# Optimization experiments

Measured on AMD Instinct MI355X. Metric: run time of the kernel, lower is better.

The kernel has to match this reference:

```python
import jax, jax.numpy as jnp
import numpy as np

ALPHA = 0.2  # LeakyReLU slope
S1, S2 = 5, 10  # neighbor sample sizes, hard-coded in the torch forward

N, F, D, C, B = 100000, 512, 256, 40, 16384


def setup_inputs() -> dict:
    key = jax.random.key(0)
    ks = jax.random.split(key, 7)
    x = jax.random.normal(ks[0], (N, F), dtype=jnp.float32)
    # xavier-like scaling for the weights
    W1 = jax.random.normal(ks[1], (D, F), dtype=jnp.float32) * (2.0 / (D + F)) ** 0.5
    W2 = jax.random.normal(ks[2], (D, D), dtype=jnp.float32) * (2.0 / (D + D)) ** 0.5
    Wc = jax.random.normal(ks[3], (C, D), dtype=jnp.float32) * (2.0 / (C + D)) ** 0.5
    nodes = jax.random.randint(ks[4], (B,), 0, N, dtype=jnp.int32)
    neigh1 = jax.random.randint(ks[5], (N, S1), 0, N, dtype=jnp.int32)
    neigh2 = jax.random.randint(ks[6], (B, S2), 0, N, dtype=jnp.int32)
    return {"x": x, "W1": W1, "W2": W2, "Wc": Wc,
            "nodes": nodes, "neigh1": neigh1, "neigh2": neigh2}


def leaky_relu(v):
    return jnp.where(v >= 0, v, ALPHA * v)


def reference(x, W1, W2, Wc, nodes, neigh1, neigh2):
    # Layer 1 (MeanAggregator, gcn=True): mean over sampled neighbors + self,
    # then linear transform + LeakyReLU. Computed for all N nodes.
    agg1 = (x[neigh1].sum(axis=1) + x) / (S1 + 1)          # [N, F]
    h1 = leaky_relu(agg1 @ W1.T)                            # [N, D]
    # Layer 2: mean over sampled neighbors + self, on batch nodes.
    agg2 = (h1[neigh2].sum(axis=1) + h1[nodes]) / (S2 + 1)  # [B, D]
    h2 = leaky_relu(agg2 @ W2.T)                            # [B, D]
    # scores = self.weight.mm(x_2.t()).t()
    scores = h2 @ Wc.T                                      # [B, C]
    return scores
```

## Files before the change

### kernel.cpp

```cpp
#include <hip/hip_runtime.h>
#include <hip/hip_bf16.h>


#define NN 100000
#define FF 512
#define DD 256
#define BB 16384
#define CC 40

typedef __attribute__((ext_vector_type(8))) short bf16x8;
typedef __attribute__((ext_vector_type(4))) float f32x4;
typedef unsigned short u16;
typedef unsigned int u32;

__device__ __forceinline__ float bf_lo(u32 u) { u32 v = u << 16; float f; __builtin_memcpy(&f, &v, 4); return f; }
__device__ __forceinline__ float bf_hi(u32 u) { u32 v = u & 0xffff0000u; float f; __builtin_memcpy(&f, &v, 4); return f; }
__device__ __forceinline__ float2 bf2f(u32 u) { return make_float2(bf_lo(u), bf_hi(u)); }
__device__ __forceinline__ u32 packbf2(float a, float b) {
  __hip_bfloat162 h = __float22bfloat162_rn(make_float2(a, b));
  u32 u; __builtin_memcpy(&u, &h, 4); return u;
}
__device__ __forceinline__ u16 fbits(float v) {
  __hip_bfloat16 h = __float2bfloat16(v);
  u16 u; __builtin_memcpy(&u, &h, 2); return u;
}
__device__ __forceinline__ float lrelu(float v) { return v >= 0.f ? v : 0.2f * v; }
__device__ __forceinline__ int swz(int r, int c) { return r * 128 + ((c ^ (r & 7)) << 4); }
__device__ __forceinline__ void gld_lds16(const u16* g, void* l) {
  __builtin_amdgcn_global_load_lds((const __attribute__((address_space(1))) unsigned int*)g,
                                   (__attribute__((address_space(3))) unsigned int*)l, 16, 0, 0);
}

__global__ __launch_bounds__(256) void k0_cvt(
    const float* __restrict__ W1, const float* __restrict__ W2, const float* __restrict__ Wc,
    u16* __restrict__ w1b, u16* __restrict__ w2b, u16* __restrict__ wcb)
{
  const int i = blockIdx.x * 256 + threadIdx.x;
  const float* src; u16* dst; int r, cc, rowE;
  if (i < 16384)      { src = W1; dst = w1b; r = i >> 6; cc = i & 63; rowE = 512; }
  else if (i < 24576) { int j = i - 16384; src = W2; dst = w2b; r = j >> 5; cc = j & 31; rowE = 256; }
  else if (i < 25856) { int j = i - 24576; src = Wc; dst = wcb; r = j >> 5; cc = j & 31; rowE = 256; }
  else return;
  const int g = cc >> 3, cp = cc & 7;
  const float* s = src + (u32)r * rowE + g * 64 + (u32)(cp ^ (r & 7)) * 8;
  const float4 v0 = *(const float4*)s;
  const float4 v1 = *(const float4*)(s + 4);
  uint4 o;
  o.x = packbf2(v0.x, v0.y); o.y = packbf2(v0.z, v0.w);
  o.z = packbf2(v1.x, v1.y); o.w = packbf2(v1.z, v1.w);
  *(uint4*)(dst + (u32)r * rowE + g * 64 + cp * 8) = o;
}

__global__ __launch_bounds__(512, 4) void k1_gemm(
    const float* __restrict__ x, const u16* __restrict__ w1b, u16* __restrict__ z)
{
  __shared__ __align__(16) unsigned char lds[49152];

  const int t = threadIdx.x;
  const int rowBase = blockIdx.x * 128;
  const int lane = t & 63, w = t >> 6;
  const int wm = w >> 2, wn = w & 3;
  const int lr = lane & 15, kg = lane >> 4;

  u32 offA[2]; int aW[2];
#pragma unroll
  for (int i = 0; i < 2; ++i) {
    const int id = t + i * 512;
    const int r = id >> 3, c = id & 7;
    int row = rowBase + r; if (row > NN - 1) row = NN - 1;
    offA[i] = (u32)row * FF + c * 8;
    aW[i] = swz(r, c);
  }
  const u32 bofs = (u32)(w * 8 + (lane >> 3)) * FF + (u32)(lane & 7) * 8;
  unsigned char* bl0 = lds + 16384 + w * 1024;

  int aA[2][4], bA[2][4];
#pragma unroll
  for (int kk = 0; kk < 2; ++kk) {
    const int cb = kk * 4 + kg;
#pragma unroll
    for (int m = 0; m < 4; ++m) aA[kk][m] = swz(wm * 64 + m * 16 + lr, cb);
#pragma unroll
    for (int n = 0; n < 4; ++n) bA[kk][n] = 16384 + swz(wn * 64 + n * 16 + lr, cb);
  }

  f32x4 acc[4][4];
#pragma unroll
  for (int m = 0; m < 4; ++m)
#pragma unroll
    for (int n = 0; n < 4; ++n) acc[m][n] = (f32x4)0.0f;

  float4 pa[2][2];
#pragma unroll
  for (int i = 0; i < 2; ++i) {
    pa[i][0] = *(const float4*)(x + offA[i]);
    pa[i][1] = *(const float4*)(x + offA[i] + 4);
  }

  for (int ks = 0; ks < 8; ++ks) {
    if (ks) __builtin_amdgcn_s_barrier();
#pragma unroll
    for (int i = 0; i < 2; ++i) {
      uint4 o;
      o.x = packbf2(pa[i][0].x, pa[i][0].y); o.y = packbf2(pa[i][0].z, pa[i][0].w);
      o.z = packbf2(pa[i][1].x, pa[i][1].y); o.w = packbf2(pa[i][1].z, pa[i][1].w);
      *(uint4*)(lds + aW[i]) = o;
    }
#pragma unroll
    for (int i = 0; i < 4; ++i)
      gld_lds16(w1b + bofs + (u32)i * 64 * FF + (u32)ks * 64, bl0 + i * 8192);
    __syncthreads();
    if (ks < 7) {
#pragma unroll
      for (int i = 0; i < 2; ++i) {
        pa[i][0] = *(const float4*)(x + offA[i] + (u32)(ks + 1) * 64);
        pa[i][1] = *(const float4*)(x + offA[i] + (u32)(ks + 1) * 64 + 4);
      }
    }
    __builtin_amdgcn_sched_barrier(0);
#pragma unroll
    for (int kk = 0; kk < 2; ++kk) {
      bf16x8 av[4], bv[4];
#pragma unroll
      for (int m = 0; m < 4; ++m) av[m] = *(const bf16x8*)(lds + aA[kk][m]);
#pragma unroll
      for (int n = 0; n < 4; ++n) bv[n] = *(const bf16x8*)(lds + bA[kk][n]);
#pragma unroll
      for (int m = 0; m < 4; ++m)
#pragma unroll
        for (int n = 0; n < 4; ++n)
          acc[m][n] = __builtin_amdgcn_mfma_f32_16x16x32_bf16(av[m], bv[n], acc[m][n], 0, 0, 0);
    }
  }
#pragma unroll
  for (int m = 0; m < 4; ++m) {
    const int r0 = rowBase + wm * 64 + m * 16 + kg * 4;
#pragma unroll
    for (int j = 0; j < 4; ++j)
#pragma unroll
      for (int n = 0; n < 4; ++n)
        z[(u32)(r0 + j) * DD + wn * 64 + n * 16 + lr] = fbits(acc[m][n][j]);
  }
}

__global__ __launch_bounds__(256) void k2_agg1(
    const u16* __restrict__ z, const int* __restrict__ neigh1, u16* __restrict__ h1)
{
  const int t = threadIdx.x;
  const int row = blockIdx.x * 8 + (t >> 5);
  const int ch = t & 31;
  const u32 o0 = (u32)row * DD + ch * 8;
  uint4 a = *(const uint4*)(z + o0);
  float2 s0 = bf2f(a.x), s1 = bf2f(a.y), s2 = bf2f(a.z), s3 = bf2f(a.w);
#pragma unroll
  for (int j = 0; j < 5; ++j) {
    const int idx = neigh1[row * 5 + j];
    const uint4 v = *(const uint4*)(z + (u32)idx * DD + ch * 8);
    s0.x += bf_lo(v.x); s0.y += bf_hi(v.x);
    s1.x += bf_lo(v.y); s1.y += bf_hi(v.y);
    s2.x += bf_lo(v.z); s2.y += bf_hi(v.z);
    s3.x += bf_lo(v.w); s3.y += bf_hi(v.w);
  }
  const float sc = 1.0f / 6.0f;
  uint4 o;
  o.x = packbf2(lrelu(s0.x * sc), lrelu(s0.y * sc));
  o.y = packbf2(lrelu(s1.x * sc), lrelu(s1.y * sc));
  o.z = packbf2(lrelu(s2.x * sc), lrelu(s2.y * sc));
  o.w = packbf2(lrelu(s3.x * sc), lrelu(s3.y * sc));
  *(uint4*)(h1 + o0) = o;
}

__global__ __launch_bounds__(512, 2) void k3_fused(
    const u16* __restrict__ h1, const u16* __restrict__ w2b, const u16* __restrict__ wcb,
    const int* __restrict__ nodes, const int* __restrict__ neigh2, float* __restrict__ out)
{
  __shared__ __align__(16) unsigned char lds[65536];

  const int t = threadIdx.x;
  const int rowBase = blockIdx.x * 64;
  const int lane = t & 63, w = t >> 6;
  const int wm = w >> 2, wn = w & 3;
  const int lr = lane & 15, kg = lane >> 4;

#pragma unroll
  for (int i = 0; i < 3; ++i) {
    const int id = t + i * 512;
    uint4 v = make_uint4(0u, 0u, 0u, 0u);
    if (id < 1280) v = *(const uint4*)(wcb + (u32)id * 8);
    *(uint4*)(lds + 40960 + id * 16) = v;
  }

  const int r = t >> 3, c = t & 7;
  const int b = rowBase + r;
  u32 offA[11];
  offA[0] = (u32)nodes[b] * DD + (u32)c * 8;
#pragma unroll
  for (int j = 0; j < 10; ++j)
    offA[1 + j] = (u32)neigh2[b * 10 + j] * DD + (u32)c * 8;
  const int aW = swz(r, c);

  const u32 bofs = (u32)(w * 8 + (lane >> 3)) * DD + (u32)(lane & 7) * 8;
  unsigned char* bl0 = lds + 8192 + w * 1024;

  int aA[2][2], bA[2][4];
#pragma unroll
  for (int kk = 0; kk < 2; ++kk) {
    const int cb = kk * 4 + kg;
#pragma unroll
    for (int m = 0; m < 2; ++m) aA[kk][m] = swz(wm * 32 + m * 16 + lr, cb);
#pragma unroll
    for (int n = 0; n < 4; ++n) bA[kk][n] = 8192 + swz(wn * 64 + n * 16 + lr, cb);
  }

  f32x4 acc[2][4];
#pragma unroll
  for (int m = 0; m < 2; ++m)
#pragma unroll
    for (int n = 0; n < 4; ++n) acc[m][n] = (f32x4)0.0f;

  uint4 ag[11];
#pragma unroll
  for (int j = 0; j < 11; ++j) ag[j] = *(const uint4*)(h1 + offA[j]);

  for (int ks = 0; ks < 4; ++ks) {
    if (ks) __builtin_amdgcn_s_barrier();
    {
      float2 s0 = make_float2(0.f, 0.f), s1 = make_float2(0.f, 0.f);
      float2 s2 = make_float2(0.f, 0.f), s3 = make_float2(0.f, 0.f);
#pragma unroll
      for (int j = 0; j < 11; ++j) {
        s0.x += bf_lo(ag[j].x); s0.y += bf_hi(ag[j].x);
        s1.x += bf_lo(ag[j].y); s1.y += bf_hi(ag[j].y);
        s2.x += bf_lo(ag[j].z); s2.y += bf_hi(ag[j].z);
        s3.x += bf_lo(ag[j].w); s3.y += bf_hi(ag[j].w);
      }
      const float sc = 1.0f / 11.0f;
      uint4 o;
      o.x = packbf2(s0.x * sc, s0.y * sc);
      o.y = packbf2(s1.x * sc, s1.y * sc);
      o.z = packbf2(s2.x * sc, s2.y * sc);
      o.w = packbf2(s3.x * sc, s3.y * sc);
      *(uint4*)(lds + aW) = o;
    }
#pragma unroll
    for (int i = 0; i < 4; ++i)
      gld_lds16(w2b + bofs + (u32)i * 64 * DD + (u32)ks * 64, bl0 + i * 8192);
    __syncthreads();
    if (ks < 3) {
#pragma unroll
      for (int j = 0; j < 11; ++j)
        ag[j] = *(const uint4*)(h1 + offA[j] + (u32)(ks + 1) * 64);
    }
    __builtin_amdgcn_sched_barrier(0);
#pragma unroll
    for (int kk = 0; kk < 2; ++kk) {
      bf16x8 av[2], bv[4];
#pragma unroll
      for (int m = 0; m < 2; ++m) av[m] = *(const bf16x8*)(lds + aA[kk][m]);
#pragma unroll
      for (int n = 0; n < 4; ++n) bv[n] = *(const bf16x8*)(lds + bA[kk][n]);
#pragma unroll
      for (int m = 0; m < 2; ++m)
#pragma unroll
        for (int n = 0; n < 4; ++n)
          acc[m][n] = __builtin_amdgcn_mfma_f32_16x16x32_bf16(av[m], bv[n], acc[m][n], 0, 0, 0);
    }
  }

  __syncthreads();
#pragma unroll
  for (int m = 0; m < 2; ++m) {
#pragma unroll
    for (int j = 0; j < 4; ++j) {
      const int row = wm * 32 + m * 16 + kg * 4 + j;
#pragma unroll
      for (int n = 0; n < 4; ++n) {
        const int col = wn * 64 + n * 16 + lr;
        const int ch = col >> 3;
        const int pch = (ch & 24) | ((ch ^ row) & 7);
        *(u16*)(lds + row * 512 + pch * 16 + (col & 7) * 2) = fbits(lrelu(acc[m][n][j]));
      }
    }
  }
  __syncthreads();

  if (w < 4) {
    f32x4 acc2[3];
#pragma unroll
    for (int n = 0; n < 3; ++n) acc2[n] = (f32x4)0.0f;
    const int arow = w * 16 + lr;
#pragma unroll
    for (int ks2 = 0; ks2 < 8; ++ks2) {
      const int chb = ks2 * 4 + kg;
      const int pchA = (chb & 24) | ((chb ^ arow) & 7);
      const bf16x8 a = *(const bf16x8*)(lds + arow * 512 + pchA * 16);
#pragma unroll
      for (int n = 0; n < 3; ++n) {
        const int brow = n * 16 + lr;
        const int pchB = (chb & 24) | ((chb ^ brow) & 7);
        const bf16x8 bb = *(const bf16x8*)(lds + 40960 + brow * 512 + pchB * 16);
        acc2[n] = __builtin_amdgcn_mfma_f32_16x16x32_bf16(a, bb, acc2[n], 0, 0, 0);
      }
    }
#pragma unroll
    for (int n = 0; n < 3; ++n) {
      const int col = n * 16 + lr;
      if (col < CC) {
#pragma unroll
        for (int j = 0; j < 4; ++j) {
          const int rr = rowBase + w * 16 + kg * 4 + j;
          out[(u32)rr * CC + col] = acc2[n][j];
        }
      }
    }
  }
}

extern "C" void kernel_launch(void* const* d_in, const int* in_sizes, int n_in,
                              void* d_out, int out_size, void* d_ws, size_t ws_size,
                              hipStream_t stream) {
  const float* x    = (const float*)d_in[0];
  const float* W1   = (const float*)d_in[1];
  const float* W2   = (const float*)d_in[2];
  const float* Wc   = (const float*)d_in[3];
  const int* nodes  = (const int*)d_in[4];
  const int* neigh1 = (const int*)d_in[5];
  const int* neigh2 = (const int*)d_in[6];

  u16* z   = (u16*)d_ws;
  u16* h1  = z + (size_t)100096 * 256;
  u16* w1b = h1 + (size_t)100096 * 256;
  u16* w2b = w1b + (size_t)256 * 512;
  u16* wcb = w2b + (size_t)256 * 256;

  k0_cvt<<<dim3(101), dim3(256), 0, stream>>>(W1, W2, Wc, w1b, w2b, wcb);
  k1_gemm<<<dim3(782), dim3(512), 0, stream>>>(x, w1b, z);
  k2_agg1<<<dim3(12500), dim3(256), 0, stream>>>(z, neigh1, h1);
  k3_fused<<<dim3(256), dim3(512), 0, stream>>>(h1, w2b, wcb, nodes, neigh2, (float*)d_out);
}
```

Before: 154.5 us.

## Double-buffer W1 tiles in LDS and vectorize GEMM output stores

The layer-1 GEMM now double-buffers the W1 tile in LDS. The next k-step's weight tile is prefetched with direct global-to-LDS loads while the current step computes, using explicit vmcnt waits and barriers in place of __syncthreads. The MFMA operand order is swapped so each lane holds four consecutive columns, which lets the output be written as packed 8-byte bf16 stores instead of scalar 2-byte stores. LDS per block grows from 48KB to 80KB, which may reduce the number of blocks resident per CU.

```diff
diff --git a/kernel.cpp b/kernel.cpp
--- a/kernel.cpp
+++ b/kernel.cpp
@@ -54,7 +54,7 @@
 __global__ __launch_bounds__(512, 4) void k1_gemm(
     const float* __restrict__ x, const u16* __restrict__ w1b, u16* __restrict__ z)
 {
-  __shared__ __align__(16) unsigned char lds[49152];
+  __shared__ __align__(16) unsigned char lds[81920];
 
   const int t = threadIdx.x;
   const int rowBase = blockIdx.x * 128;
@@ -72,7 +72,6 @@
     aW[i] = swz(r, c);
   }
   const u32 bofs = (u32)(w * 8 + (lane >> 3)) * FF + (u32)(lane & 7) * 8;
-  unsigned char* bl0 = lds + 16384 + w * 1024;
 
   int aA[2][4], bA[2][4];
 #pragma unroll
@@ -96,9 +95,16 @@
     pa[i][0] = *(const float4*)(x + offA[i]);
     pa[i][1] = *(const float4*)(x + offA[i] + 4);
   }
-
+#pragma unroll
+  for (int i = 0; i < 4; ++i)
+    gld_lds16(w1b + bofs + (u32)i * 64 * FF, lds + 16384 + w * 1024 + i * 8192);
+
+#pragma unroll
   for (int ks = 0; ks < 8; ++ks) {
-    if (ks) __builtin_amdgcn_s_barrier();
+    if (ks) {
+      __builtin_amdgcn_s_barrier();
+      __builtin_amdgcn_sched_barrier(0);
+    }
 #pragma unroll
     for (int i = 0; i < 2; ++i) {
       uint4 o;
@@ -106,40 +112,49 @@
       o.z = packbf2(pa[i][1].x, pa[i][1].y); o.w = packbf2(pa[i][1].z, pa[i][1].w);
       *(uint4*)(lds + aW[i]) = o;
     }
-#pragma unroll
-    for (int i = 0; i < 4; ++i)
-      gld_lds16(w1b + bofs + (u32)i * 64 * FF + (u32)ks * 64, bl0 + i * 8192);
-    __syncthreads();
     if (ks < 7) {
 #pragma unroll
       for (int i = 0; i < 2; ++i) {
         pa[i][0] = *(const float4*)(x + offA[i] + (u32)(ks + 1) * 64);
         pa[i][1] = *(const float4*)(x + offA[i] + (u32)(ks + 1) * 64 + 4);
       }
+      unsigned char* bl = lds + 16384 + ((ks + 1) & 1) * 32768 + w * 1024;
+#pragma unroll
+      for (int i = 0; i < 4; ++i)
+        gld_lds16(w1b + bofs + (u32)i * 64 * FF + (u32)(ks + 1) * 64, bl + i * 8192);
+      asm volatile("s_waitcnt vmcnt(8) lgkmcnt(0)" ::: "memory");
+    } else {
+      asm volatile("s_waitcnt vmcnt(0) lgkmcnt(0)" ::: "memory");
     }
     __builtin_amdgcn_sched_barrier(0);
+    __builtin_amdgcn_s_barrier();
+    __builtin_amdgcn_sched_barrier(0);
+    const int bo = (ks & 1) * 32768;
 #pragma unroll
     for (int kk = 0; kk < 2; ++kk) {
       bf16x8 av[4], bv[4];
 #pragma unroll
       for (int m = 0; m < 4; ++m) av[m] = *(const bf16x8*)(lds + aA[kk][m]);
 #pragma unroll
-      for (int n = 0; n < 4; ++n) bv[n] = *(const bf16x8*)(lds + bA[kk][n]);
+      for (int n = 0; n < 4; ++n) bv[n] = *(const bf16x8*)(lds + bA[kk][n] + bo);
 #pragma unroll
       for (int m = 0; m < 4; ++m)
 #pragma unroll
         for (int n = 0; n < 4; ++n)
-          acc[m][n] = __builtin_amdgcn_mfma_f32_16x16x32_bf16(av[m], bv[n], acc[m][n], 0, 0, 0);
+          acc[m][n] = __builtin_amdgcn_mfma_f32_16x16x32_bf16(bv[n], av[m], acc[m][n], 0, 0, 0);
     }
   }
 #pragma unroll
   for (int m = 0; m < 4; ++m) {
-    const int r0 = rowBase + wm * 64 + m * 16 + kg * 4;
-#pragma unroll
-    for (int j = 0; j < 4; ++j)
-#pragma unroll
-      for (int n = 0; n < 4; ++n)
-        z[(u32)(r0 + j) * DD + wn * 64 + n * 16 + lr] = fbits(acc[m][n][j]);
+    const u32 zr = (u32)(rowBase + wm * 64 + m * 16 + lr);
+#pragma unroll
+    for (int n = 0; n < 4; ++n) {
+      const int zc = wn * 64 + n * 16 + kg * 4;
+      uint2 o;
+      o.x = packbf2(acc[m][n][0], acc[m][n][1]);
+      o.y = packbf2(acc[m][n][2], acc[m][n][3]);
+      *(uint2*)(z + zr * DD + zc) = o;
+    }
   }
 }
 
```

New measurement: 152.1 us. No clear change (-1.5%).
